# Kernel optimization log

Measured on AMD Instinct MI355X. Metric: run time of the kernel, lower is better.

Reference implementation:

```python
import jax, jax.numpy as jnp
import numpy as np
import math

DIM = 1536
NH = 12
HD = 128          # head_dim
C = HD // 2       # 64 complex rope dims
MAX_ATTN = 15 * 880
EPS = 1e-6


def _rope_tables(max_len=1024, d=HD, theta=10000.0):
    # Wan rope_params: freqs = cat([rope(1024, d-4*(d//6)), rope(1024, 2*(d//6)), rope(1024, 2*(d//6))], dim=1)
    d0 = d - 4 * (d // 6)   # 44 -> 22 complex dims (F axis)
    d1 = 2 * (d // 6)       # 42 -> 21 complex dims (H and W axes)
    parts = []
    for dd in (d0, d1, d1):
        inv = 1.0 / theta ** (np.arange(0, dd, 2, dtype=np.float32) / dd)
        parts.append(np.outer(np.arange(max_len, dtype=np.float32), inv))
    ang = np.concatenate(parts, axis=1)                 # [1024, C]
    return np.stack([np.cos(ang), np.sin(ang)], -1)     # [1024, C, 2]


def rmsnorm(x, g, eps=EPS):
    return x * jax.lax.rsqrt(jnp.mean(x * x, axis=-1, keepdims=True) + eps) * g


def rope_apply(xq, f, h, w, freqs, start_frame):
    # xq: [B, S, N, D]; freqs: [1024, C, 2] cos/sin tables; S = f*h*w
    b, s, n, d = xq.shape
    c = d // 2
    s0 = c - 2 * (c // 3)   # F-axis complex dims (22)
    s1 = c // 3             # H/W-axis complex dims (21)
    cos, sin = freqs[..., 0], freqs[..., 1]

    def per_token(tab):
        tf = jnp.broadcast_to(tab[start_frame:start_frame + f, :s0][:, None, None, :], (f, h, w, s0))
        th = jnp.broadcast_to(tab[:h, s0:s0 + s1][None, :, None, :], (f, h, w, s1))
        tw = jnp.broadcast_to(tab[:w, s0 + s1:][None, None, :, :], (f, h, w, s1))
        return jnp.concatenate([tf, th, tw], -1).reshape(1, s, 1, c)

    pc, ps = per_token(cos), per_token(sin)
    xr = xq.reshape(b, s, n, c, 2)
    re, im = xr[..., 0], xr[..., 1]
    out = jnp.stack([re * pc - im * ps, re * ps + im * pc], -1)
    return out.reshape(b, s, n, d)


def _forward(x, wq, bq, wk, bk, wv, bv, wo, bo, gq, gk, freqs, k_cache, v_cache, f, h, w, current_start):
    b, s, _ = x.shape
    frame_seqlen = h * w
    start_frame = current_start // frame_seqlen

    q = rmsnorm(x @ wq.T + bq, gq).reshape(b, s, NH, HD)
    k = rmsnorm(x @ wk.T + bk, gk).reshape(b, s, NH, HD)
    v = (x @ wv.T + bv).reshape(b, s, NH, HD)

    rq = rope_apply(q, f, h, w, freqs, start_frame)
    rk = rope_apply(k, f, h, w, freqs, start_frame)

    current_end = current_start + s
    # cache not full: append new keys/values at [current_start:current_end]
    k_cache = jax.lax.dynamic_update_slice(k_cache, rk, (0, current_start, 0, 0))
    v_cache = jax.lax.dynamic_update_slice(v_cache, v, (0, current_start, 0, 0))

    win_start = max(0, current_end - MAX_ATTN)
    kk = k_cache[:, win_start:current_end]   # [B, Lk, N, D]
    vv = v_cache[:, win_start:current_end]

    scale = 1.0 / math.sqrt(HD)
    scores = jnp.einsum('bqnd,bknd->bnqk', rq, kk) * scale
    attn = jax.nn.softmax(scores, axis=-1)
    out = jnp.einsum('bnqk,bknd->bqnd', attn, vv).reshape(b, s, DIM)
    return out @ wo.T + bo


def setup_inputs() -> dict:
    key = jax.random.key(0)
    ks = jax.random.split(key, 8)
    B, S, CACHE = 1, 880, 18 * 880
    x = jax.random.normal(ks[0], (B, S, DIM), jnp.float32)

    def lin(k):
        k1, k2 = jax.random.split(k)
        wgt = jax.random.normal(k1, (DIM, DIM), jnp.float32) / math.sqrt(DIM)
        bia = jax.random.normal(k2, (DIM,), jnp.float32) * 0.01
        return wgt, bia

    wq, bq = lin(ks[1]); wk, bk = lin(ks[2]); wv, bv = lin(ks[3]); wo, bo = lin(ks[4])
    gq = jnp.ones((DIM,), jnp.float32)
    gk = jnp.ones((DIM,), jnp.float32)
    freqs = jnp.asarray(_rope_tables())
    k_cache = jax.random.normal(ks[5], (B, CACHE, NH, HD), jnp.float32) * 0.5
    v_cache = jax.random.normal(ks[6], (B, CACHE, NH, HD), jnp.float32) * 0.5
    grid_sizes = jnp.array([1, 22, 40], jnp.int32)  # (F, H, W), H*W = 880
    return dict(x=x, wq=wq, bq=bq, wk=wk, bk=bk, wv=wv, bv=bv, wo=wo, bo=bo,
                gq=gq, gk=gk, freqs=freqs, k_cache=k_cache, v_cache=v_cache,
                grid_sizes=grid_sizes, current_start=10560)


def reference(x, wq, bq, wk, bk, wv, bv, wo, bo, gq, gk, freqs, k_cache, v_cache, grid_sizes, current_start):
    f, h, w = (int(grid_sizes[0]), int(grid_sizes[1]), int(grid_sizes[2]))
    return _forward(x, wq, bq, wk, bk, wv, bv, wo, bo, gq, gk, freqs,
                    k_cache, v_cache, f, h, w, int(current_start))
```

## Files before the change

kernel.cpp:

```cpp
#include <hip/hip_runtime.h>

#define NHEADS 12
#define HDIM 128
#define MODEL_DIM 1536
#define MAX_ATTN_W 13200
#define NSPLIT 12

typedef unsigned short u16;
typedef unsigned int u32;
typedef float f32x4 __attribute__((ext_vector_type(4)));
typedef float f32x16 __attribute__((ext_vector_type(16)));
typedef __bf16 bf16x8 __attribute__((ext_vector_type(8)));

static __device__ __forceinline__ u16 f2bf(float f) {
  union { __bf16 h; u16 u; } cv;
  cv.h = (__bf16)f;
  return cv.u;
}
static __device__ __forceinline__ float bf2f(u16 u) {
  union { u32 u; float f; } cv;
  cv.u = ((u32)u) << 16;
  return cv.f;
}

__global__ void k_conv_bf16(const float* __restrict__ src, u16* __restrict__ dst, int n4) {
  int i = blockIdx.x * blockDim.x + threadIdx.x;
  if (i >= n4) return;
  float4 v = ((const float4*)src)[i];
  u32 lo = (u32)f2bf(v.x) | ((u32)f2bf(v.y) << 16);
  u32 hi = (u32)f2bf(v.z) | ((u32)f2bf(v.w) << 16);
  ((uint2*)dst)[i] = make_uint2(lo, hi);
}

__global__ void k_conv_bf16_w4(const float* __restrict__ s0, const float* __restrict__ s1,
                               const float* __restrict__ s2, const float* __restrict__ s3,
                               u16* __restrict__ d0, u16* __restrict__ d1,
                               u16* __restrict__ d2, u16* __restrict__ d3, int n4) {
  int i = blockIdx.x * blockDim.x + threadIdx.x;
  if (i >= n4) return;
  const int which = blockIdx.y;
  const float* src = (which == 0) ? s0 : (which == 1) ? s1 : (which == 2) ? s2 : s3;
  u16* dst = (which == 0) ? d0 : (which == 1) ? d1 : (which == 2) ? d2 : d3;
  float4 v = ((const float4*)src)[i];
  u32 lo = (u32)f2bf(v.x) | ((u32)f2bf(v.y) << 16);
  u32 hi = (u32)f2bf(v.z) | ((u32)f2bf(v.w) << 16);
  ((uint2*)dst)[i] = make_uint2(lo, hi);
}

__global__ void k_build_kold(const float* __restrict__ kc, u16* __restrict__ K_all,
                             const int* __restrict__ csp, int S, int KVcap) {
  const int cs = csp[0];
  const int ce = cs + S;
  int wst = ce - MAX_ATTN_W; if (wst < 0) wst = 0;
  const int oldlen = cs - wst;
  const long per = (long)oldlen * 16;
  const long total = per * NHEADS;
  for (long c = blockIdx.x * (long)blockDim.x + threadIdx.x; c < total;
       c += (long)gridDim.x * blockDim.x) {
    int n = (int)(c / per);
    long r = c - (long)n * per;
    int jo = (int)(r >> 4);
    int dc = ((int)r & 15) * 8;
    const float* s = kc + ((size_t)(wst + jo) * NHEADS + n) * HDIM + dc;
    float4 a = *(const float4*)s;
    float4 b = *(const float4*)(s + 4);
    uint4 o;
    o.x = (u32)f2bf(a.x) | ((u32)f2bf(a.y) << 16);
    o.y = (u32)f2bf(a.z) | ((u32)f2bf(a.w) << 16);
    o.z = (u32)f2bf(b.x) | ((u32)f2bf(b.y) << 16);
    o.w = (u32)f2bf(b.z) | ((u32)f2bf(b.w) << 16);
    *(uint4*)(K_all + ((size_t)n * KVcap + jo) * HDIM + dc) = o;
  }
}

__launch_bounds__(256)
__global__ void k_build_vtold(const float* __restrict__ vc, u16* __restrict__ VT,
                              const int* __restrict__ csp, int S, int KVcap) {
  __shared__ u16 tile[64][130];
  const int cs = csp[0];
  const int ce = cs + S;
  int wst = ce - MAX_ATTN_W; if (wst < 0) wst = 0;
  const int oldlen = cs - wst;
  const int n = blockIdx.y;
  const int j0 = blockIdx.x * 64;
  if (j0 >= oldlen) return;
  const int tid = threadIdx.x;

  #pragma unroll
  for (int i = 0; i < 8; i++) {
    int idx = tid + 256 * i;
    int j = idx >> 5;
    int dc = (idx & 31) * 4;
    float4 v = make_float4(0.f, 0.f, 0.f, 0.f);
    if (j0 + j < oldlen)
      v = *(const float4*)(vc + ((size_t)(wst + j0 + j) * NHEADS + n) * HDIM + dc);
    u32 lo = (u32)f2bf(v.x) | ((u32)f2bf(v.y) << 16);
    u32 hi = (u32)f2bf(v.z) | ((u32)f2bf(v.w) << 16);
    *(u32*)&tile[j][dc] = lo;
    *(u32*)&tile[j][dc + 2] = hi;
  }
  __syncthreads();

  const int d = tid >> 1;
  const int jh = (tid & 1) * 32;
  alignas(16) u16 buf[32];
  #pragma unroll
  for (int j = 0; j < 32; j++) buf[j] = tile[jh + j][d];
  u16* dst = VT + ((size_t)n * HDIM + d) * KVcap + j0 + jh;
  if (j0 + jh + 32 <= oldlen) {
    #pragma unroll
    for (int c = 0; c < 4; c++)
      *(uint4*)(dst + c * 8) = *(const uint4*)&buf[c * 8];
  } else {
    for (int j = 0; j < 32 && j0 + jh + j < oldlen; j++) dst[j] = buf[j];
  }
}

__launch_bounds__(256)
__global__ void k_gemm_bt(const u16* __restrict__ A, const u16* __restrict__ B,
                          const float* __restrict__ bias, float* __restrict__ out,
                          int M, int N, int K) {
  __shared__ __align__(16) u16 Al[64][40];
  __shared__ __align__(16) u16 Bl[64][40];
  const int tid = threadIdx.x;
  const int w = tid >> 6, l = tid & 63, l15 = l & 15, g = l >> 4;
  const int wr = w >> 1, wc = w & 1;
  const int m0 = blockIdx.x * 64, n0 = blockIdx.y * 64;
  f32x4 acc[2][2] = {};
  const int row = tid >> 2, colc = (tid & 3) * 8;
  for (int k0 = 0; k0 < K; k0 += 32) {
    __syncthreads();
    uint4 av = make_uint4(0, 0, 0, 0);
    int gm = m0 + row;
    if (gm < M) av = *(const uint4*)(A + (size_t)gm * K + k0 + colc);
    *(uint4*)&Al[row][colc] = av;
    uint4 bv = *(const uint4*)(B + (size_t)(n0 + row) * K + k0 + colc);
    *(uint4*)&Bl[row][colc] = bv;
    __syncthreads();
    bf16x8 af[2], bfr[2];
    #pragma unroll
    for (int mt = 0; mt < 2; mt++) af[mt] = *(const bf16x8*)&Al[wr * 32 + mt * 16 + l15][g * 8];
    #pragma unroll
    for (int nt = 0; nt < 2; nt++) bfr[nt] = *(const bf16x8*)&Bl[wc * 32 + nt * 16 + l15][g * 8];
    #pragma unroll
    for (int mt = 0; mt < 2; mt++)
      #pragma unroll
      for (int nt = 0; nt < 2; nt++)
        acc[mt][nt] = __builtin_amdgcn_mfma_f32_16x16x32_bf16(af[mt], bfr[nt], acc[mt][nt], 0, 0, 0);
  }
  #pragma unroll
  for (int mt = 0; mt < 2; mt++)
    #pragma unroll
    for (int nt = 0; nt < 2; nt++)
      #pragma unroll
      for (int r = 0; r < 4; r++) {
        int mm = m0 + wr * 32 + mt * 16 + (g << 2) + r;
        int nn = n0 + wc * 32 + nt * 16 + l15;
        if (mm < M) out[(size_t)mm * N + nn] = acc[mt][nt][r] + bias[nn];
      }
}

__launch_bounds__(256)
__global__ void k_gemm_qkv128(const u16* __restrict__ A,
                              const u16* __restrict__ B0, const u16* __restrict__ B1,
                              const u16* __restrict__ B2,
                              const float* __restrict__ bias0, const float* __restrict__ bias1,
                              const float* __restrict__ bias2,
                              float* __restrict__ o0, float* __restrict__ o1, float* __restrict__ o2,
                              int M, int N, int K) {
  __shared__ __align__(16) u16 Al[128][40];
  __shared__ __align__(16) u16 Bl[128][40];
  const int nblk = N / 128;
  const int which = blockIdx.y / nblk;
  const int n0 = (blockIdx.y % nblk) * 128;
  const u16* B = (which == 0) ? B0 : ((which == 1) ? B1 : B2);
  const float* bias = (which == 0) ? bias0 : ((which == 1) ? bias1 : bias2);
  float* out = (which == 0) ? o0 : ((which == 1) ? o1 : o2);
  const int tid = threadIdx.x;
  const int wid = tid >> 6, l = tid & 63, l31 = l & 31, hi = l >> 5;
  const int wr = wid >> 1, wc = wid & 1;
  const int m0 = blockIdx.x * 128;
  f32x16 acc[2][2];
  #pragma unroll
  for (int mt = 0; mt < 2; mt++)
    #pragma unroll
    for (int nt = 0; nt < 2; nt++)
      #pragma unroll
      for (int j = 0; j < 16; j++) acc[mt][nt][j] = 0.f;
  const int row = tid >> 2, colc = (tid & 3) * 8;
  for (int k0 = 0; k0 < K; k0 += 32) {
    __syncthreads();
    uint4 a0 = *(const uint4*)(A + (size_t)(m0 + row) * K + k0 + colc);
    uint4 a1 = *(const uint4*)(A + (size_t)(m0 + row + 64) * K + k0 + colc);
    uint4 b0 = *(const uint4*)(B + (size_t)(n0 + row) * K + k0 + colc);
    uint4 b1 = *(const uint4*)(B + (size_t)(n0 + row + 64) * K + k0 + colc);
    *(uint4*)&Al[row][colc] = a0;
    *(uint4*)&Al[row + 64][colc] = a1;
    *(uint4*)&Bl[row][colc] = b0;
    *(uint4*)&Bl[row + 64][colc] = b1;
    __syncthreads();
    #pragma unroll
    for (int ks = 0; ks < 2; ks++) {
      bf16x8 af[2], bfr[2];
      #pragma unroll
      for (int mt = 0; mt < 2; mt++)
        af[mt] = *(const bf16x8*)&Al[wr * 64 + mt * 32 + l31][ks * 16 + hi * 8];
      #pragma unroll
      for (int nt = 0; nt < 2; nt++)
        bfr[nt] = *(const bf16x8*)&Bl[wc * 64 + nt * 32 + l31][ks * 16 + hi * 8];
      #pragma unroll
      for (int mt = 0; mt < 2; mt++)
        #pragma unroll
        for (int nt = 0; nt < 2; nt++)
          acc[mt][nt] = __builtin_amdgcn_mfma_f32_32x32x16_bf16(af[mt], bfr[nt], acc[mt][nt], 0, 0, 0);
    }
  }
  #pragma unroll
  for (int mt = 0; mt < 2; mt++)
    #pragma unroll
    for (int nt = 0; nt < 2; nt++) {
      const int col = n0 + wc * 64 + nt * 32 + l31;
      const float bb = bias[col];
      #pragma unroll
      for (int r = 0; r < 16; r++) {
        int rowo = m0 + wr * 64 + mt * 32 + (r & 3) + 8 * (r >> 2) + 4 * hi;
        if (rowo < M) out[(size_t)rowo * N + col] = acc[mt][nt][r] + bb;
      }
    }
}

__launch_bounds__(256)
__global__ void k_norm_rope(const float* __restrict__ qp, const float* __restrict__ kp,
                            const float* __restrict__ vp, const float* __restrict__ gq,
                            const float* __restrict__ gk, const float* __restrict__ freqs,
                            const int* __restrict__ gs, const int* __restrict__ csp,
                            int S, int KVcap,
                            u16* __restrict__ rq, u16* __restrict__ K_all,
                            u16* __restrict__ VT) {
  const int t = blockIdx.x;
  const int tid = threadIdx.x;
  const float* q = qp + (size_t)t * MODEL_DIM;
  const float* k = kp + (size_t)t * MODEL_DIM;
  const float* v = vp + (size_t)t * MODEL_DIM;
  float sq = 0.f, sk = 0.f;
  for (int j = tid; j < MODEL_DIM; j += 256) {
    float a = q[j]; sq += a * a;
    float b = k[j]; sk += b * b;
  }
  #pragma unroll
  for (int off = 32; off > 0; off >>= 1) {
    sq += __shfl_down(sq, off, 64);
    sk += __shfl_down(sk, off, 64);
  }
  __shared__ float red[8];
  int wv_ = tid >> 6, l = tid & 63;
  if (l == 0) { red[wv_] = sq; red[4 + wv_] = sk; }
  __syncthreads();
  sq = red[0] + red[1] + red[2] + red[3];
  sk = red[4] + red[5] + red[6] + red[7];
  const float rq_s = rsqrtf(sq * (1.0f / MODEL_DIM) + 1e-6f) * 0.12751744f;
  const float rk_s = rsqrtf(sk * (1.0f / MODEL_DIM) + 1e-6f);

  const int cs = csp[0];
  const int h = gs[1], ww = gs[2];
  const int hw = h * ww;
  const int sf = cs / hw;
  const int fi = t / hw;
  const int rr = t - fi * hw;
  const int hi = rr / ww;
  const int wi = rr - hi * ww;
  const int ce = cs + S;
  int wst = ce - MAX_ATTN_W; if (wst < 0) wst = 0;
  const int jj = cs + t - wst;

  for (int p = tid; p < NHEADS * 64; p += 256) {
    int n = p >> 6, c = p & 63;
    int pos = (c < 22) ? (sf + fi) : ((c < 43) ? hi : wi);
    float cv = freqs[(pos * 64 + c) * 2];
    float sv = freqs[(pos * 64 + c) * 2 + 1];
    int j0 = n * HDIM + 2 * c;
    float qr = q[j0] * rq_s * gq[j0];
    float qi = q[j0 + 1] * rq_s * gq[j0 + 1];
    u32 oq = (u32)f2bf(qr * cv - qi * sv) | ((u32)f2bf(qr * sv + qi * cv) << 16);
    *(u32*)(rq + ((size_t)n * S + t) * HDIM + 2 * c) = oq;
    float kr = k[j0] * rk_s * gk[j0];
    float ki = k[j0 + 1] * rk_s * gk[j0 + 1];
    u32 ok = (u32)f2bf(kr * cv - ki * sv) | ((u32)f2bf(kr * sv + ki * cv) << 16);
    *(u32*)(K_all + ((size_t)n * KVcap + jj) * HDIM + 2 * c) = ok;
  }
  for (int j = tid; j < MODEL_DIM; j += 256) {
    int n = j >> 7, d = j & 127;
    VT[((size_t)n * HDIM + d) * KVcap + jj] = f2bf(v[j]);
  }
}

__launch_bounds__(256, 2)
__global__ void k_attn_split(const u16* __restrict__ rq, const u16* __restrict__ K_all,
                             const u16* __restrict__ VT,
                             u16* __restrict__ po, float* __restrict__ pm, float* __restrict__ pl,
                             const int* __restrict__ csp, int S, int KVcap) {
  __shared__ __align__(16) u16 Klds[64][128];
  __shared__ __align__(16) u16 Vlds[128][64];

  const int tid = threadIdx.x;
  const int wid = tid >> 6;
  const int l = tid & 63;
  const int l31 = l & 31;
  const int hi = l >> 5;
  const int swz = (l31 & 7) << 3;
  const int head = blockIdx.y;
  const int split = blockIdx.z;
  const int q0 = blockIdx.x * 128;

  const int cs = csp[0];
  const int ce = cs + S;
  int wst = ce - MAX_ATTN_W; if (wst < 0) wst = 0;
  const int KV = ce - wst;
  const int chunk = (((KV + NSPLIT - 1) / NSPLIT) + 63) & ~63;
  const int kstart = split * chunk;
  int kend = kstart + chunk; if (kend > KV) kend = KV;

  const size_t pbase = ((size_t)head * NSPLIT + split) * S;
  const int qrow = q0 + wid * 32 + l31;

  if (kstart >= kend) {
    if (qrow < S && hi == 0) { pm[pbase + qrow] = -3.0e38f; pl[pbase + qrow] = 0.f; }
    return;
  }

  bf16x8 qf[8];
  if (qrow < S) {
    const u16* qp = rq + ((size_t)head * S + qrow) * HDIM;
    #pragma unroll
    for (int ds = 0; ds < 8; ds++) qf[ds] = *(const bf16x8*)(qp + ds * 16 + hi * 8);
  } else {
    #pragma unroll
    for (int ds = 0; ds < 8; ds++)
      #pragma unroll
      for (int i = 0; i < 8; i++) qf[ds][i] = (__bf16)0.0f;
  }

  f32x16 o[4];
  #pragma unroll
  for (int dt = 0; dt < 4; dt++)
    #pragma unroll
    for (int j = 0; j < 16; j++) o[dt][j] = 0.f;
  float m_ = -3.0e38f, lsum_ = 0.f;

  const u16* Kh = K_all + (size_t)head * KVcap * HDIM;
  const u16* Vh = VT + (size_t)head * HDIM * KVcap;

  uint4 kr[4], vr[4];
  auto load_tile = [&](int key0) {
    #pragma unroll
    for (int i = 0; i < 4; i++) {
      int cid = tid + 256 * i;
      int krow = cid >> 4;
      int gk_ = key0 + krow;
      kr[i] = make_uint4(0, 0, 0, 0);
      if (gk_ < kend) kr[i] = *(const uint4*)(Kh + (size_t)gk_ * HDIM + (cid & 15) * 8);
    }
    #pragma unroll
    for (int i = 0; i < 4; i++) {
      int cid = tid + 256 * i;
      int d = cid >> 3;
      int kc = (cid & 7) * 8;
      const u16* src = Vh + (size_t)d * KVcap + key0 + kc;
      if (key0 + kc + 8 <= kend) {
        vr[i] = *(const uint4*)src;
      } else {
        alignas(16) u16 tmp[8];
        #pragma unroll
        for (int j = 0; j < 8; j++) tmp[j] = (key0 + kc + j < kend) ? src[j] : (u16)0;
        vr[i] = *(const uint4*)tmp;
      }
    }
  };

  const int ntiles = (kend - kstart + 63) >> 6;
  load_tile(kstart);

  for (int t = 0; t < ntiles; t++) {
    const int key0 = kstart + (t << 6);
    __syncthreads();
    #pragma unroll
    for (int i = 0; i < 4; i++) {
      int cid = tid + 256 * i;
      int krow = cid >> 4;
      *(uint4*)&Klds[krow][((cid & 15) * 8) ^ ((krow & 7) << 3)] = kr[i];
    }
    #pragma unroll
    for (int i = 0; i < 4; i++) {
      int cid = tid + 256 * i;
      int d = cid >> 3;
      *(uint4*)&Vlds[d][((cid & 7) * 8) ^ ((d & 7) << 3)] = vr[i];
    }
    if (t + 1 < ntiles) load_tile(key0 + 64);
    __syncthreads();

    f32x16 s[2];
    #pragma unroll
    for (int kt = 0; kt < 2; kt++) {
      #pragma unroll
      for (int j = 0; j < 16; j++) s[kt][j] = 0.f;
      #pragma unroll
      for (int ds = 0; ds < 8; ds++) {
        bf16x8 kf = *(const bf16x8*)&Klds[kt * 32 + l31][(ds * 16 + hi * 8) ^ swz];
        s[kt] = __builtin_amdgcn_mfma_f32_32x32x16_bf16(kf, qf[ds], s[kt], 0, 0, 0);
      }
    }

    float tm = -3.0e38f;
    if (key0 + 64 <= kend) {
      #pragma unroll
      for (int kt = 0; kt < 2; kt++)
        #pragma unroll
        for (int r = 0; r < 16; r++) tm = fmaxf(tm, s[kt][r]);
    } else {
      #pragma unroll
      for (int kt = 0; kt < 2; kt++) {
        const int rem = kend - key0 - kt * 32;
        #pragma unroll
        for (int r = 0; r < 16; r++) {
          const int off = (r & 3) + 8 * (r >> 2) + 4 * hi;
          float v = (off < rem) ? s[kt][r] : -3.0e38f;
          s[kt][r] = v;
          tm = fmaxf(tm, v);
        }
      }
    }
    tm = fmaxf(tm, __shfl_xor(tm, 32, 64));

    if (!__all(tm <= m_ + 8.0f)) {
      float nm = fmaxf(m_, tm);
      float alpha = exp2f(m_ - nm);
      m_ = nm;
      lsum_ *= alpha;
      #pragma unroll
      for (int dt = 0; dt < 4; dt++)
        #pragma unroll
        for (int j = 0; j < 16; j++) o[dt][j] *= alpha;
    }

    float rs = 0.f;
    u32 w[2][8];
    #pragma unroll
    for (int kt = 0; kt < 2; kt++)
      #pragma unroll
      for (int j = 0; j < 8; j++) {
        float p0 = exp2f(s[kt][2 * j] - m_);
        float p1 = exp2f(s[kt][2 * j + 1] - m_);
        rs += p0 + p1;
        w[kt][j] = (u32)f2bf(p0) | ((u32)f2bf(p1) << 16);
      }
    rs += __shfl_xor(rs, 32, 64);
    lsum_ += rs;

    union { u32 u[4]; bf16x8 v; } pf[2][2];
    #pragma unroll
    for (int kt = 0; kt < 2; kt++) {
      u32 xw[8];
      #pragma unroll
      for (int j = 0; j < 8; j++) xw[j] = __shfl_xor(w[kt][j], 32, 64);
      pf[kt][0].u[0] = hi ? xw[2]    : w[kt][0];
      pf[kt][0].u[1] = hi ? xw[3]    : w[kt][1];
      pf[kt][0].u[2] = hi ? w[kt][2] : xw[0];
      pf[kt][0].u[3] = hi ? w[kt][3] : xw[1];
      pf[kt][1].u[0] = hi ? xw[6]    : w[kt][4];
      pf[kt][1].u[1] = hi ? xw[7]    : w[kt][5];
      pf[kt][1].u[2] = hi ? w[kt][6] : xw[4];
      pf[kt][1].u[3] = hi ? w[kt][7] : xw[5];
    }

    #pragma unroll
    for (int dt = 0; dt < 4; dt++) {
      #pragma unroll
      for (int kt = 0; kt < 2; kt++)
        #pragma unroll
        for (int mm = 0; mm < 2; mm++) {
          bf16x8 vf = *(const bf16x8*)&Vlds[dt * 32 + l31][(kt * 32 + mm * 16 + hi * 8) ^ swz];
          o[dt] = __builtin_amdgcn_mfma_f32_32x32x16_bf16(vf, pf[kt][mm].v, o[dt], 0, 0, 0);
        }
    }
  }

  if (qrow < S) {
    float rl = (lsum_ > 0.f) ? (1.0f / lsum_) : 0.f;
    u16* dst = po + (pbase + qrow) * HDIM;
    #pragma unroll
    for (int dt = 0; dt < 4; dt++)
      #pragma unroll
      for (int jj = 0; jj < 4; jj++) {
        u32 w0 = (u32)f2bf(o[dt][4 * jj] * rl) | ((u32)f2bf(o[dt][4 * jj + 1] * rl) << 16);
        u32 w1 = (u32)f2bf(o[dt][4 * jj + 2] * rl) | ((u32)f2bf(o[dt][4 * jj + 3] * rl) << 16);
        *(uint2*)(dst + dt * 32 + 8 * jj + 4 * hi) = make_uint2(w0, w1);
      }
    if (hi == 0) { pm[pbase + qrow] = m_; pl[pbase + qrow] = lsum_; }
  }
}

__global__ void k_attn_reduce(const u16* __restrict__ po, const float* __restrict__ pm,
                              const float* __restrict__ pl, u16* __restrict__ attn_out,
                              int S) {
  const int t = blockIdx.x;
  const int h = blockIdx.y;
  const int d = threadIdx.x;
  float ms[NSPLIT];
  float M = -3.0e38f;
  #pragma unroll
  for (int s = 0; s < NSPLIT; s++) {
    ms[s] = pm[((size_t)h * NSPLIT + s) * S + t];
    M = fmaxf(M, ms[s]);
  }
  float L = 0.f, acc = 0.f;
  #pragma unroll
  for (int s = 0; s < NSPLIT; s++) {
    float wgt = exp2f(ms[s] - M) * pl[((size_t)h * NSPLIT + s) * S + t];
    L += wgt;
    acc += wgt * bf2f(po[(((size_t)h * NSPLIT + s) * S + t) * HDIM + d]);
  }
  attn_out[(size_t)t * MODEL_DIM + h * HDIM + d] = f2bf(acc / L);
}

extern "C" void kernel_launch(void* const* d_in, const int* in_sizes, int n_in,
                              void* d_out, int out_size, void* d_ws, size_t ws_size,
                              hipStream_t stream) {
  (void)n_in; (void)out_size; (void)ws_size;
  const float* x  = (const float*)d_in[0];
  const float* wq = (const float*)d_in[1];
  const float* bq = (const float*)d_in[2];
  const float* wk = (const float*)d_in[3];
  const float* bk = (const float*)d_in[4];
  const float* wv = (const float*)d_in[5];
  const float* bv = (const float*)d_in[6];
  const float* wo = (const float*)d_in[7];
  const float* bo = (const float*)d_in[8];
  const float* gq = (const float*)d_in[9];
  const float* gk = (const float*)d_in[10];
  const float* freqs = (const float*)d_in[11];
  const float* k_cache = (const float*)d_in[12];
  const float* v_cache = (const float*)d_in[13];
  const int* gs  = (const int*)d_in[14];
  const int* csp = (const int*)d_in[15];

  const int S = in_sizes[0] / MODEL_DIM;
  const int CACHE = in_sizes[12] / (NHEADS * HDIM);
  const int KVcap = (CACHE < MAX_ATTN_W) ? CACHE : MAX_ATTN_W;
  const int Mpad = (S + 127) & ~127;

  char* ws = (char*)d_ws;
  size_t off = 0;
  auto alloc = [&](size_t bytes) {
    char* p = ws + off;
    off += (bytes + 255) & ~(size_t)255;
    return p;
  };
  u16* xb   = (u16*)alloc((size_t)Mpad * MODEL_DIM * 2);
  u16* wqb  = (u16*)alloc((size_t)MODEL_DIM * MODEL_DIM * 2);
  u16* wkb  = (u16*)alloc((size_t)MODEL_DIM * MODEL_DIM * 2);
  u16* wvb  = (u16*)alloc((size_t)MODEL_DIM * MODEL_DIM * 2);
  u16* wob  = (u16*)alloc((size_t)MODEL_DIM * MODEL_DIM * 2);
  float* q_pre = (float*)alloc((size_t)S * MODEL_DIM * 4);
  float* k_pre = (float*)alloc((size_t)S * MODEL_DIM * 4);
  float* v_pre = (float*)alloc((size_t)S * MODEL_DIM * 4);
  u16* rqb   = (u16*)alloc((size_t)NHEADS * S * HDIM * 2);
  u16* K_all = (u16*)alloc((size_t)NHEADS * KVcap * HDIM * 2);
  u16* VT    = (u16*)alloc((size_t)NHEADS * HDIM * KVcap * 2);
  u16* attn_o = (u16*)alloc((size_t)S * MODEL_DIM * 2);
  u16* po    = (u16*)alloc((size_t)NHEADS * NSPLIT * S * HDIM * 2);
  float* pm  = (float*)alloc((size_t)NHEADS * NSPLIT * S * 4);
  float* pl  = (float*)alloc((size_t)NHEADS * NSPLIT * S * 4);

  const int nx4 = S * MODEL_DIM / 4;
  const int nw4 = MODEL_DIM * MODEL_DIM / 4;
  hipLaunchKernelGGL(k_conv_bf16, dim3((nx4 + 255) / 256), dim3(256), 0, stream, x, xb, nx4);
  hipLaunchKernelGGL(k_conv_bf16_w4, dim3((nw4 + 255) / 256, 4), dim3(256), 0, stream,
                     wq, wk, wv, wo, wqb, wkb, wvb, wob, nw4);

  hipLaunchKernelGGL(k_build_kold, dim3(2048), dim3(256), 0, stream, k_cache, K_all, csp, S, KVcap);
  hipLaunchKernelGGL(k_build_vtold, dim3((KVcap + 63) / 64, NHEADS), dim3(256), 0, stream,
                     v_cache, VT, csp, S, KVcap);

  hipLaunchKernelGGL(k_gemm_qkv128, dim3(Mpad / 128, 3 * MODEL_DIM / 128), dim3(256), 0, stream,
                     xb, wqb, wkb, wvb, bq, bk, bv, q_pre, k_pre, v_pre, S, MODEL_DIM, MODEL_DIM);

  hipLaunchKernelGGL(k_norm_rope, dim3(S), dim3(256), 0, stream,
                     q_pre, k_pre, v_pre, gq, gk, freqs, gs, csp, S, KVcap, rqb, K_all, VT);

  hipLaunchKernelGGL(k_attn_split, dim3((S + 127) / 128, NHEADS, NSPLIT), dim3(256), 0, stream,
                     rqb, K_all, VT, po, pm, pl, csp, S, KVcap);

  hipLaunchKernelGGL(k_attn_reduce, dim3(S, NHEADS), dim3(128), 0, stream, po, pm, pl, attn_o, S);

  hipLaunchKernelGGL(k_gemm_bt, dim3((S + 63) / 64, MODEL_DIM / 64), dim3(256), 0, stream,
                     attn_o, wob, bo, (float*)d_out, S, MODEL_DIM, MODEL_DIM);
}
```

Baseline: 323.1 us.

## Double-buffer attention K/V tiles in LDS and widen output-projection GEMM tiles

The split attention kernel now keeps two LDS buffers for K and V, so the next tile is written to shared memory while the current one feeds the MFMAs, and it prefetches two tiles ahead. This removes one barrier per tile and hides global-load latency. The MFMA sections are wrapped in s_setprio to favour matrix issue. The output projection GEMM moves from 64x64 tiles using 16x16 MFMA to 128x128 tiles using 32x32x16 MFMA, which raises data reuse. In exchange it pads attn_o to Mpad and drops the row bound check on A loads, and doubling LDS may lower attention occupancy.

Result: slower. 333.6 us (+3.3%).

```diff
diff --git a/kernel.cpp b/kernel.cpp
--- a/kernel.cpp
+++ b/kernel.cpp
@@ -117,47 +117,63 @@
 }
 
 __launch_bounds__(256)
-__global__ void k_gemm_bt(const u16* __restrict__ A, const u16* __restrict__ B,
-                          const float* __restrict__ bias, float* __restrict__ out,
-                          int M, int N, int K) {
-  __shared__ __align__(16) u16 Al[64][40];
-  __shared__ __align__(16) u16 Bl[64][40];
+__global__ void k_gemm_o128(const u16* __restrict__ A, const u16* __restrict__ B,
+                            const float* __restrict__ bias, float* __restrict__ out,
+                            int M, int N, int K) {
+  __shared__ __align__(16) u16 Al[128][40];
+  __shared__ __align__(16) u16 Bl[128][40];
+  const int n0 = blockIdx.y * 128;
   const int tid = threadIdx.x;
-  const int w = tid >> 6, l = tid & 63, l15 = l & 15, g = l >> 4;
-  const int wr = w >> 1, wc = w & 1;
-  const int m0 = blockIdx.x * 64, n0 = blockIdx.y * 64;
-  f32x4 acc[2][2] = {};
+  const int wid = tid >> 6, l = tid & 63, l31 = l & 31, hi = l >> 5;
+  const int wr = wid >> 1, wc = wid & 1;
+  const int m0 = blockIdx.x * 128;
+  f32x16 acc[2][2];
+  #pragma unroll
+  for (int mt = 0; mt < 2; mt++)
+    #pragma unroll
+    for (int nt = 0; nt < 2; nt++)
+      #pragma unroll
+      for (int j = 0; j < 16; j++) acc[mt][nt][j] = 0.f;
   const int row = tid >> 2, colc = (tid & 3) * 8;
   for (int k0 = 0; k0 < K; k0 += 32) {
     __syncthreads();
-    uint4 av = make_uint4(0, 0, 0, 0);
-    int gm = m0 + row;
-    if (gm < M) av = *(const uint4*)(A + (size_t)gm * K + k0 + colc);
-    *(uint4*)&Al[row][colc] = av;
-    uint4 bv = *(const uint4*)(B + (size_t)(n0 + row) * K + k0 + colc);
-    *(uint4*)&Bl[row][colc] = bv;
+    uint4 a0 = *(const uint4*)(A + (size_t)(m0 + row) * K + k0 + colc);
+    uint4 a1 = *(const uint4*)(A + (size_t)(m0 + row + 64) * K + k0 + colc);
+    uint4 b0 = *(const uint4*)(B + (size_t)(n0 + row) * K + k0 + colc);
+    uint4 b1 = *(const uint4*)(B + (size_t)(n0 + row + 64) * K + k0 + colc);
+    *(uint4*)&Al[row][colc] = a0;
+    *(uint4*)&Al[row + 64][colc] = a1;
+    *(uint4*)&Bl[row][colc] = b0;
+    *(uint4*)&Bl[row + 64][colc] = b1;
     __syncthreads();
-    bf16x8 af[2], bfr[2];
-    #pragma unroll
-    for (int mt = 0; mt < 2; mt++) af[mt] = *(const bf16x8*)&Al[wr * 32 + mt * 16 + l15][g * 8];
-    #pragma unroll
-    for (int nt = 0; nt < 2; nt++) bfr[nt] = *(const bf16x8*)&Bl[wc * 32 + nt * 16 + l15][g * 8];
-    #pragma unroll
-    for (int mt = 0; mt < 2; mt++)
+    #pragma unroll
+    for (int ks = 0; ks < 2; ks++) {
+      bf16x8 af[2], bfr[2];
+      #pragma unroll
+      for (int mt = 0; mt < 2; mt++)
+        af[mt] = *(const bf16x8*)&Al[wr * 64 + mt * 32 + l31][ks * 16 + hi * 8];
       #pragma unroll
       for (int nt = 0; nt < 2; nt++)
-        acc[mt][nt] = __builtin_amdgcn_mfma_f32_16x16x32_bf16(af[mt], bfr[nt], acc[mt][nt], 0, 0, 0);
+        bfr[nt] = *(const bf16x8*)&Bl[wc * 64 + nt * 32 + l31][ks * 16 + hi * 8];
+      #pragma unroll
+      for (int mt = 0; mt < 2; mt++)
+        #pragma unroll
+        for (int nt = 0; nt < 2; nt++)
+          acc[mt][nt] = __builtin_amdgcn_mfma_f32_32x32x16_bf16(af[mt], bfr[nt], acc[mt][nt], 0, 0, 0);
+    }
   }
   #pragma unroll
   for (int mt = 0; mt < 2; mt++)
     #pragma unroll
-    for (int nt = 0; nt < 2; nt++)
-      #pragma unroll
-      for (int r = 0; r < 4; r++) {
-        int mm = m0 + wr * 32 + mt * 16 + (g << 2) + r;
-        int nn = n0 + wc * 32 + nt * 16 + l15;
-        if (mm < M) out[(size_t)mm * N + nn] = acc[mt][nt][r] + bias[nn];
+    for (int nt = 0; nt < 2; nt++) {
+      const int col = n0 + wc * 64 + nt * 32 + l31;
+      const float bb = bias[col];
+      #pragma unroll
+      for (int r = 0; r < 16; r++) {
+        int rowo = m0 + wr * 64 + mt * 32 + (r & 3) + 8 * (r >> 2) + 4 * hi;
+        if (rowo < M) out[(size_t)rowo * N + col] = acc[mt][nt][r] + bb;
       }
+    }
 }
 
 __launch_bounds__(256)
@@ -299,8 +315,8 @@
                              const u16* __restrict__ VT,
                              u16* __restrict__ po, float* __restrict__ pm, float* __restrict__ pl,
                              const int* __restrict__ csp, int S, int KVcap) {
-  __shared__ __align__(16) u16 Klds[64][128];
-  __shared__ __align__(16) u16 Vlds[128][64];
+  __shared__ __align__(16) u16 Klds[2][64][128];
+  __shared__ __align__(16) u16 Vlds[2][128][64];
 
   const int tid = threadIdx.x;
   const int wid = tid >> 6;
@@ -376,39 +392,46 @@
       }
     }
   };
-
-  const int ntiles = (kend - kstart + 63) >> 6;
-  load_tile(kstart);
-
-  for (int t = 0; t < ntiles; t++) {
-    const int key0 = kstart + (t << 6);
-    __syncthreads();
+  auto stage_to = [&](int p) {
     #pragma unroll
     for (int i = 0; i < 4; i++) {
       int cid = tid + 256 * i;
       int krow = cid >> 4;
-      *(uint4*)&Klds[krow][((cid & 15) * 8) ^ ((krow & 7) << 3)] = kr[i];
+      *(uint4*)&Klds[p][krow][((cid & 15) * 8) ^ ((krow & 7) << 3)] = kr[i];
     }
     #pragma unroll
     for (int i = 0; i < 4; i++) {
       int cid = tid + 256 * i;
       int d = cid >> 3;
-      *(uint4*)&Vlds[d][((cid & 7) * 8) ^ ((d & 7) << 3)] = vr[i];
-    }
-    if (t + 1 < ntiles) load_tile(key0 + 64);
+      *(uint4*)&Vlds[p][d][((cid & 7) * 8) ^ ((d & 7) << 3)] = vr[i];
+    }
+  };
+
+  const int ntiles = (kend - kstart + 63) >> 6;
+  load_tile(kstart);
+  stage_to(0);
+  if (ntiles > 1) load_tile(kstart + 64);
+
+  for (int t = 0; t < ntiles; t++) {
+    const int key0 = kstart + (t << 6);
+    const int cur = t & 1;
     __syncthreads();
+    if (t + 1 < ntiles) stage_to(cur ^ 1);
+    if (t + 2 < ntiles) load_tile(key0 + 128);
 
     f32x16 s[2];
+    __builtin_amdgcn_s_setprio(1);
     #pragma unroll
     for (int kt = 0; kt < 2; kt++) {
       #pragma unroll
       for (int j = 0; j < 16; j++) s[kt][j] = 0.f;
       #pragma unroll
       for (int ds = 0; ds < 8; ds++) {
-        bf16x8 kf = *(const bf16x8*)&Klds[kt * 32 + l31][(ds * 16 + hi * 8) ^ swz];
+        bf16x8 kf = *(const bf16x8*)&Klds[cur][kt * 32 + l31][(ds * 16 + hi * 8) ^ swz];
         s[kt] = __builtin_amdgcn_mfma_f32_32x32x16_bf16(kf, qf[ds], s[kt], 0, 0, 0);
       }
     }
+    __builtin_amdgcn_s_setprio(0);
 
     float tm = -3.0e38f;
     if (key0 + 64 <= kend) {
@@ -472,16 +495,18 @@
       pf[kt][1].u[3] = hi ? w[kt][7] : xw[5];
     }
 
+    __builtin_amdgcn_s_setprio(1);
     #pragma unroll
     for (int dt = 0; dt < 4; dt++) {
       #pragma unroll
       for (int kt = 0; kt < 2; kt++)
         #pragma unroll
         for (int mm = 0; mm < 2; mm++) {
-          bf16x8 vf = *(const bf16x8*)&Vlds[dt * 32 + l31][(kt * 32 + mm * 16 + hi * 8) ^ swz];
+          bf16x8 vf = *(const bf16x8*)&Vlds[cur][dt * 32 + l31][(kt * 32 + mm * 16 + hi * 8) ^ swz];
           o[dt] = __builtin_amdgcn_mfma_f32_32x32x16_bf16(vf, pf[kt][mm].v, o[dt], 0, 0, 0);
         }
     }
+    __builtin_amdgcn_s_setprio(0);
   }
 
   if (qrow < S) {
@@ -566,7 +591,7 @@
   u16* rqb   = (u16*)alloc((size_t)NHEADS * S * HDIM * 2);
   u16* K_all = (u16*)alloc((size_t)NHEADS * KVcap * HDIM * 2);
   u16* VT    = (u16*)alloc((size_t)NHEADS * HDIM * KVcap * 2);
-  u16* attn_o = (u16*)alloc((size_t)S * MODEL_DIM * 2);
+  u16* attn_o = (u16*)alloc((size_t)Mpad * MODEL_DIM * 2);
   u16* po    = (u16*)alloc((size_t)NHEADS * NSPLIT * S * HDIM * 2);
   float* pm  = (float*)alloc((size_t)NHEADS * NSPLIT * S * 4);
   float* pl  = (float*)alloc((size_t)NHEADS * NSPLIT * S * 4);
@@ -592,6 +617,6 @@
 
   hipLaunchKernelGGL(k_attn_reduce, dim3(S, NHEADS), dim3(128), 0, stream, po, pm, pl, attn_o, S);
 
-  hipLaunchKernelGGL(k_gemm_bt, dim3((S + 63) / 64, MODEL_DIM / 64), dim3(256), 0, stream,
+  hipLaunchKernelGGL(k_gemm_o128, dim3(Mpad / 128, MODEL_DIM / 128), dim3(256), 0, stream,
                      attn_o, wob, bo, (float*)d_out, S, MODEL_DIM, MODEL_DIM);
 }
```
